# Optimization experiments

Measured on AMD Instinct MI355X. Metric: run time of the kernel, lower is better.

The kernel has to match this reference:

```python
import jax, jax.numpy as jnp
import numpy as np

B, S, HID = 4, 4096, 1024
NUM_HEADS, HEAD_DIM = 16, 64  # HID // NUM_HEADS
EPS = 1e-8  # torch F.cosine_similarity eps


def setup_inputs() -> dict:
    key = jax.random.key(0)
    ks = jax.random.split(key, 12)
    scale = 1.0 / np.sqrt(HID)
    d = {
        "query": jax.random.normal(ks[0], (B, S, HID), jnp.float32),
        "key": jax.random.normal(ks[1], (B, S, HID), jnp.float32),
        "value": jax.random.normal(ks[2], (B, S, HID), jnp.float32),
        "Wq": jax.random.normal(ks[3], (HID, HID), jnp.float32) * scale,
        "bq": jnp.zeros((HID,), jnp.float32),
        "Wk": jax.random.normal(ks[4], (HID, HID), jnp.float32) * scale,
        "bk": jnp.zeros((HID,), jnp.float32),
        "Wv": jax.random.normal(ks[5], (HID, HID), jnp.float32) * scale,
        "bv": jnp.zeros((HID,), jnp.float32),
        "Wo": jax.random.normal(ks[6], (HID, HID), jnp.float32) * scale,
        "bo": jnp.zeros((HID,), jnp.float32),
        "score_weights": jax.random.normal(ks[7], (3,), jnp.float32),
    }
    return d


def reference(query, key, value, Wq, bq, Wk, bk, Wv, bv, Wo, bo, score_weights):
    # Projections; NOTE: original reshapes to (B, S, H, D) and never transposes,
    # so all attention scores are over the HEADS axis (shape (B,S,H,H)).
    q = (query @ Wq + bq).reshape(B, S, NUM_HEADS, HEAD_DIM)
    k = (key @ Wk + bk).reshape(B, S, NUM_HEADS, HEAD_DIM)
    v = (value @ Wv + bv).reshape(B, S, NUM_HEADS, HEAD_DIM)

    # Shared inner products between heads at each (b, s): (B, S, H, H)
    qk = jnp.einsum('bsqd,bskd->bsqk', q, k)

    # 1) scaled dot product
    dot = qk / jnp.sqrt(jnp.float32(HEAD_DIM))

    # 2) cosine similarity (F.cosine_similarity with eps=1e-8)
    qn = jnp.linalg.norm(q, axis=-1)  # (B,S,H)
    kn = jnp.linalg.norm(k, axis=-1)
    cos = qk / jnp.maximum(qn[..., :, None] * kn[..., None, :], EPS)

    # 3) negative Euclidean distance (torch.cdist, p=2)
    sq = jnp.sum(q * q, axis=-1)  # (B,S,H)
    sk = jnp.sum(k * k, axis=-1)
    dist2 = jnp.maximum(sq[..., :, None] + sk[..., None, :] - 2.0 * qk, 0.0)
    dist = -jnp.sqrt(dist2)

    w = jax.nn.softmax(score_weights)
    scores = w[0] * dot + w[1] * cos + w[2] * dist  # (B,S,H,H)

    attention = jax.nn.softmax(scores, axis=-1)  # dropout = identity (eval)
    out = jnp.einsum('bsqk,bskd->bsqd', attention, v)  # (B,S,H,D)

    # Faithful to torch: transpose(1,2) -> (B,H,S,D), then view (B, S, HID)
    out = out.transpose(0, 2, 1, 3).reshape(B, S, HID)
    return out @ Wo + bo, attention
```

## Files before the change

kernel.cpp:

```cpp
#include <hip/hip_runtime.h>
#include <stdint.h>

#define BB 4
#define SS 4096
#define HID 1024
#define NH 16
#define HD 64
#define TOKENS (BB * SS)

typedef unsigned short u16;
typedef __bf16 bf16x8 __attribute__((ext_vector_type(8)));
typedef float f32x4 __attribute__((ext_vector_type(4)));
typedef __attribute__((address_space(1))) unsigned int u32g;
typedef __attribute__((address_space(3))) unsigned int u32l;

__device__ __forceinline__ u16 f2bf(float f) {
  union { float f; unsigned u; } v; v.f = f;
  unsigned u = v.u;
  unsigned r = u + 0x7fffu + ((u >> 16) & 1u);
  return (u16)(r >> 16);
}
__device__ __forceinline__ float bf2f(u16 h) {
  union { unsigned u; float f; } v; v.u = ((unsigned)h) << 16;
  return v.f;
}

__device__ __forceinline__ void async16(const void* g, void* l) {
  __builtin_amdgcn_global_load_lds((const u32g*)g, (u32l*)l, 16, 0, 0);
}

__global__ __launch_bounds__(256) void cast3_bf16(
    const float* __restrict__ q, const float* __restrict__ k,
    const float* __restrict__ v, u16* __restrict__ qo, u16* __restrict__ ko,
    u16* __restrict__ vo) {
  const int z = blockIdx.z;
  const float* s = (z == 0) ? q : (z == 1) ? k : v;
  u16* d = (z == 0) ? qo : (z == 1) ? ko : vo;
  size_t i = ((size_t)blockIdx.x * 256 + threadIdx.x) * 8;
  float4 f0 = *(const float4*)(s + i);
  float4 f1 = *(const float4*)(s + i + 4);
  ushort4 h0, h1;
  h0.x = f2bf(f0.x); h0.y = f2bf(f0.y); h0.z = f2bf(f0.z); h0.w = f2bf(f0.w);
  h1.x = f2bf(f1.x); h1.y = f2bf(f1.y); h1.z = f2bf(f1.z); h1.w = f2bf(f1.w);
  *(ushort4*)(d + i) = h0;
  *(ushort4*)(d + i + 4) = h1;
}

__global__ __launch_bounds__(256) void transpose_cast4(
    const float* __restrict__ W0, const float* __restrict__ W1,
    const float* __restrict__ W2, const float* __restrict__ W3,
    u16* __restrict__ T0, u16* __restrict__ T1, u16* __restrict__ T2,
    u16* __restrict__ T3) {
  const int z = blockIdx.z;
  const float* W = (z == 0) ? W0 : (z == 1) ? W1 : (z == 2) ? W2 : W3;
  u16* Wt = (z == 0) ? T0 : (z == 1) ? T1 : (z == 2) ? T2 : T3;
  __shared__ float t[32][33];
  const int bx = blockIdx.x * 32;
  const int by = blockIdx.y * 32;
  const int x = threadIdx.x;
#pragma unroll
  for (int yy = threadIdx.y; yy < 32; yy += 8)
    t[yy][x] = W[(size_t)(by + yy) * HID + bx + x];
  __syncthreads();
#pragma unroll
  for (int yy = threadIdx.y; yy < 32; yy += 8)
    Wt[(size_t)(bx + yy) * HID + by + x] = f2bf(t[x][yy]);
}

template <bool C_BF16, int NZ>
__global__ __launch_bounds__(256, 4) void gemm_bt(
    const u16* __restrict__ A0, const u16* __restrict__ A1,
    const u16* __restrict__ A2, const u16* __restrict__ B0,
    const u16* __restrict__ B1, const u16* __restrict__ B2,
    const float* __restrict__ bias0, const float* __restrict__ bias1,
    const float* __restrict__ bias2, void* __restrict__ C0,
    void* __restrict__ C1, void* __restrict__ C2, int M, int N, int K) {
  const u16* A = A0;
  const u16* Bt = B0;
  const float* bias = bias0;
  void* Cv = C0;
  if (NZ > 1) {
    int z = blockIdx.z;
    A = (z == 0) ? A0 : (z == 1) ? A1 : A2;
    Bt = (z == 0) ? B0 : (z == 1) ? B1 : B2;
    bias = (z == 0) ? bias0 : (z == 1) ? bias1 : bias2;
    Cv = (z == 0) ? C0 : (z == 1) ? C1 : C2;
  }
  __shared__ u16 As[128 * 32];
  __shared__ u16 Bs[128 * 32];
  const int tid = threadIdx.x;
  const int wave = tid >> 6, lane = tid & 63;
  const int quad = lane >> 4, l16 = lane & 15;
  const int m0 = blockIdx.x * 128, n0 = blockIdx.y * 128;
  const int wm = (wave >> 1) * 64, wn = (wave & 1) * 64;

  f32x4 acc[4][4] = {};

  for (int kt = 0; kt < K; kt += 32) {
    __syncthreads();
    {
      const u16* srcB = Bt + (size_t)n0 * K + kt;
      const u16* srcA = A + (size_t)m0 * K + kt;
#pragma unroll
      for (int is = 0; is < 2; ++is) {
        int g = is * 256 + wave * 64 + lane;
        const u16* gpB = srcB + (size_t)(g >> 2) * K + (g & 3) * 8;
        const u16* gpA = srcA + (size_t)(g >> 2) * K + (g & 3) * 8;
        async16(gpB, &Bs[(is * 256 + wave * 64) * 8]);
        async16(gpA, &As[(is * 256 + wave * 64) * 8]);
      }
    }
    __syncthreads();
    bf16x8 af[4], bfr[4];
#pragma unroll
    for (int i = 0; i < 4; ++i)
      af[i] = *(const bf16x8*)&As[(wm + i * 16 + l16) * 32 + quad * 8];
#pragma unroll
    for (int j = 0; j < 4; ++j)
      bfr[j] = *(const bf16x8*)&Bs[(wn + j * 16 + l16) * 32 + quad * 8];
#pragma unroll
    for (int i = 0; i < 4; ++i)
#pragma unroll
      for (int j = 0; j < 4; ++j)
        acc[i][j] = __builtin_amdgcn_mfma_f32_16x16x32_bf16(af[i], bfr[j],
                                                            acc[i][j], 0, 0, 0);
  }

  const int cb = n0 + wn + l16;
#pragma unroll
  for (int i = 0; i < 4; ++i) {
    int rowb = m0 + wm + i * 16 + quad * 4;
#pragma unroll
    for (int j = 0; j < 4; ++j) {
      int col = cb + j * 16;
      float bv = bias[col];
#pragma unroll
      for (int r = 0; r < 4; ++r) {
        float v = acc[i][j][r] + bv;
        if (C_BF16)
          ((u16*)Cv)[(size_t)(rowb + r) * N + col] = f2bf(v);
        else
          ((float*)Cv)[(size_t)(rowb + r) * N + col] = v;
      }
    }
  }
}

__global__ __launch_bounds__(256, 4) void attention_kernel(
    const u16* __restrict__ qb, const u16* __restrict__ kb,
    const u16* __restrict__ vb, const float* __restrict__ sw,
    float* __restrict__ attn_out, u16* __restrict__ o) {
  __shared__ float qs[16][65], ks[16][65], vs[16][65];
  __shared__ float sq[16], sk[16], qn[16], kn[16];
  __shared__ float attn_s[16][17];
  const int tid = threadIdx.x;
  const int token = blockIdx.x;
  const size_t base = (size_t)token * HID;

  {
    int idx = tid * 4;
    int h = idx >> 6, d = idx & 63;
    ushort4 uq = *(const ushort4*)(qb + base + idx);
    ushort4 uk = *(const ushort4*)(kb + base + idx);
    ushort4 uv = *(const ushort4*)(vb + base + idx);
    qs[h][d] = bf2f(uq.x); qs[h][d + 1] = bf2f(uq.y);
    qs[h][d + 2] = bf2f(uq.z); qs[h][d + 3] = bf2f(uq.w);
    ks[h][d] = bf2f(uk.x); ks[h][d + 1] = bf2f(uk.y);
    ks[h][d + 2] = bf2f(uk.z); ks[h][d + 3] = bf2f(uk.w);
    vs[h][d] = bf2f(uv.x); vs[h][d + 1] = bf2f(uv.y);
    vs[h][d + 2] = bf2f(uv.z); vs[h][d + 3] = bf2f(uv.w);
  }
  __syncthreads();

  if (tid < 32) {
    int i = tid & 15;
    const float* row = (tid < 16) ? qs[i] : ks[i];
    float s = 0.f;
#pragma unroll
    for (int d = 0; d < 64; ++d) s += row[d] * row[d];
    if (tid < 16) { sq[i] = s; qn[i] = sqrtf(s); }
    else          { sk[i] = s; kn[i] = sqrtf(s); }
  }
  __syncthreads();

  float s0 = sw[0], s1 = sw[1], s2 = sw[2];
  float smx = fmaxf(s0, fmaxf(s1, s2));
  float e0 = expf(s0 - smx), e1 = expf(s1 - smx), e2 = expf(s2 - smx);
  float winv = 1.f / (e0 + e1 + e2);
  float w0 = e0 * winv, w1 = e1 * winv, w2 = e2 * winv;

  const int i = tid >> 4, j = tid & 15;
  float attn;
  {
    float dot = 0.f;
#pragma unroll
    for (int d = 0; d < 64; ++d) dot += qs[i][d] * ks[j][d];
    float sdot = dot * 0.125f;
    float cosv = dot / fmaxf(qn[i] * kn[j], 1e-8f);
    float d2 = fmaxf(sq[i] + sk[j] - 2.f * dot, 0.f);
    float dist = -sqrtf(d2);
    float score = w0 * sdot + w1 * cosv + w2 * dist;
    float mx = score;
#pragma unroll
    for (int off = 8; off; off >>= 1) mx = fmaxf(mx, __shfl_xor(mx, off, 16));
    float e = expf(score - mx);
    float sum = e;
#pragma unroll
    for (int off = 8; off; off >>= 1) sum += __shfl_xor(sum, off, 16);
    attn = e / sum;
  }
  attn_out[(size_t)token * 256 + tid] = attn;
  attn_s[i][j] = attn;
  __syncthreads();

  {
    int d0 = j * 4;
    float o0 = 0.f, o1 = 0.f, o2 = 0.f, o3 = 0.f;
#pragma unroll
    for (int jj = 0; jj < 16; ++jj) {
      float a = attn_s[i][jj];
      o0 += a * vs[jj][d0];
      o1 += a * vs[jj][d0 + 1];
      o2 += a * vs[jj][d0 + 2];
      o3 += a * vs[jj][d0 + 3];
    }
    int b = token >> 12, s = token & (SS - 1);
    size_t off = (size_t)b * (SS * HID) + (size_t)i * (SS * HD) +
                 (size_t)s * HD + d0;
    ushort4 h;
    h.x = f2bf(o0); h.y = f2bf(o1); h.z = f2bf(o2); h.w = f2bf(o3);
    *(ushort4*)(o + off) = h;
  }
}

extern "C" void kernel_launch(void* const* d_in, const int* in_sizes, int n_in,
                              void* d_out, int out_size, void* d_ws,
                              size_t ws_size, hipStream_t stream) {
  (void)in_sizes; (void)n_in; (void)out_size; (void)ws_size;
  const float* query = (const float*)d_in[0];
  const float* key_  = (const float*)d_in[1];
  const float* value = (const float*)d_in[2];
  const float* Wq = (const float*)d_in[3];
  const float* bq = (const float*)d_in[4];
  const float* Wk = (const float*)d_in[5];
  const float* bk = (const float*)d_in[6];
  const float* Wv = (const float*)d_in[7];
  const float* bv = (const float*)d_in[8];
  const float* Wo = (const float*)d_in[9];
  const float* bo = (const float*)d_in[10];
  const float* sw = (const float*)d_in[11];

  char* ws = (char*)d_ws;
  u16* Wqt = (u16*)ws; ws += (size_t)HID * HID * 2;
  u16* Wkt = (u16*)ws; ws += (size_t)HID * HID * 2;
  u16* Wvt = (u16*)ws; ws += (size_t)HID * HID * 2;
  u16* Wot = (u16*)ws; ws += (size_t)HID * HID * 2;
  u16* qh = (u16*)ws; ws += (size_t)TOKENS * HID * 2;
  u16* kh = (u16*)ws; ws += (size_t)TOKENS * HID * 2;
  u16* vh = (u16*)ws; ws += (size_t)TOKENS * HID * 2;
  u16* qb = (u16*)ws; ws += (size_t)TOKENS * HID * 2;
  u16* kb = (u16*)ws; ws += (size_t)TOKENS * HID * 2;
  u16* vb = (u16*)ws; ws += (size_t)TOKENS * HID * 2;
  u16* ob = (u16*)ws; ws += (size_t)TOKENS * HID * 2;

  float* out0 = (float*)d_out;
  float* attn_out = out0 + (size_t)TOKENS * HID;

  transpose_cast4<<<dim3(32, 32, 4), dim3(32, 8), 0, stream>>>(
      Wq, Wk, Wv, Wo, Wqt, Wkt, Wvt, Wot);

  cast3_bf16<<<dim3(TOKENS * HID / (256 * 8), 1, 3), 256, 0, stream>>>(
      query, key_, value, qh, kh, vh);

  gemm_bt<true, 3><<<dim3(TOKENS / 128, HID / 128, 3), 256, 0, stream>>>(
      qh, kh, vh, Wqt, Wkt, Wvt, bq, bk, bv, qb, kb, vb, TOKENS, HID, HID);

  attention_kernel<<<TOKENS, 256, 0, stream>>>(qb, kb, vb, sw, attn_out, ob);

  gemm_bt<false, 1><<<dim3(TOKENS / 128, HID / 128, 1), 256, 0, stream>>>(
      ob, nullptr, nullptr, Wot, nullptr, nullptr, bo, nullptr, nullptr,
      out0, nullptr, nullptr, TOKENS, HID, HID);
}
```

Before: 506.7 us.

## Fuse input cast into QKV GEMM, swizzle LDS, MFMA-based per-token attention

Drops the separate fp32-to-bf16 cast kernel. The QKV GEMM now loads fp32 activations directly, converts them to bf16 in registers and writes them into XOR-swizzled LDS. Both GEMMs use the swizzled LDS layout to reduce bank conflicts. Attention processes four tokens per block, one per wave, computing the head-by-head QK product with MFMA and reusing the loaded fragments for the norms. It also uses fast exp and vectorized output stores. The trade-off is that the A tile is no longer loaded asynchronously into LDS, so global loads sit on the GEMM's critical path, and fast exp slightly changes numerics.

```diff
diff --git a/kernel.cpp b/kernel.cpp
--- a/kernel.cpp
+++ b/kernel.cpp
@@ -10,6 +10,7 @@
 
 typedef unsigned short u16;
 typedef __bf16 bf16x8 __attribute__((ext_vector_type(8)));
+typedef u16 u16x8 __attribute__((ext_vector_type(8)));
 typedef float f32x4 __attribute__((ext_vector_type(4)));
 typedef __attribute__((address_space(1))) unsigned int u32g;
 typedef __attribute__((address_space(3))) unsigned int u32l;
@@ -24,26 +25,12 @@
   union { unsigned u; float f; } v; v.u = ((unsigned)h) << 16;
   return v.f;
 }
+__device__ __forceinline__ unsigned pack2(float a, float b) {
+  return (unsigned)f2bf(a) | ((unsigned)f2bf(b) << 16);
+}
 
 __device__ __forceinline__ void async16(const void* g, void* l) {
   __builtin_amdgcn_global_load_lds((const u32g*)g, (u32l*)l, 16, 0, 0);
-}
-
-__global__ __launch_bounds__(256) void cast3_bf16(
-    const float* __restrict__ q, const float* __restrict__ k,
-    const float* __restrict__ v, u16* __restrict__ qo, u16* __restrict__ ko,
-    u16* __restrict__ vo) {
-  const int z = blockIdx.z;
-  const float* s = (z == 0) ? q : (z == 1) ? k : v;
-  u16* d = (z == 0) ? qo : (z == 1) ? ko : vo;
-  size_t i = ((size_t)blockIdx.x * 256 + threadIdx.x) * 8;
-  float4 f0 = *(const float4*)(s + i);
-  float4 f1 = *(const float4*)(s + i + 4);
-  ushort4 h0, h1;
-  h0.x = f2bf(f0.x); h0.y = f2bf(f0.y); h0.z = f2bf(f0.z); h0.w = f2bf(f0.w);
-  h1.x = f2bf(f1.x); h1.y = f2bf(f1.y); h1.z = f2bf(f1.z); h1.w = f2bf(f1.w);
-  *(ushort4*)(d + i) = h0;
-  *(ushort4*)(d + i + 4) = h1;
 }
 
 __global__ __launch_bounds__(256) void transpose_cast4(
@@ -67,25 +54,21 @@
     Wt[(size_t)(bx + yy) * HID + by + x] = f2bf(t[x][yy]);
 }
 
-template <bool C_BF16, int NZ>
-__global__ __launch_bounds__(256, 4) void gemm_bt(
-    const u16* __restrict__ A0, const u16* __restrict__ A1,
-    const u16* __restrict__ A2, const u16* __restrict__ B0,
+
+__global__ __launch_bounds__(256, 4) void gemm_qkv(
+    const float* __restrict__ A0, const float* __restrict__ A1,
+    const float* __restrict__ A2, const u16* __restrict__ B0,
     const u16* __restrict__ B1, const u16* __restrict__ B2,
     const float* __restrict__ bias0, const float* __restrict__ bias1,
-    const float* __restrict__ bias2, void* __restrict__ C0,
-    void* __restrict__ C1, void* __restrict__ C2, int M, int N, int K) {
-  const u16* A = A0;
-  const u16* Bt = B0;
-  const float* bias = bias0;
-  void* Cv = C0;
-  if (NZ > 1) {
-    int z = blockIdx.z;
-    A = (z == 0) ? A0 : (z == 1) ? A1 : A2;
-    Bt = (z == 0) ? B0 : (z == 1) ? B1 : B2;
-    bias = (z == 0) ? bias0 : (z == 1) ? bias1 : bias2;
-    Cv = (z == 0) ? C0 : (z == 1) ? C1 : C2;
-  }
+    const float* __restrict__ bias2, u16* __restrict__ C0,
+    u16* __restrict__ C1, u16* __restrict__ C2) {
+  const int z = blockIdx.z;
+  const float* A = (z == 0) ? A0 : (z == 1) ? A1 : A2;
+  const u16* Bt = (z == 0) ? B0 : (z == 1) ? B1 : B2;
+  const float* bias = (z == 0) ? bias0 : (z == 1) ? bias1 : bias2;
+  u16* Cv = (z == 0) ? C0 : (z == 1) ? C1 : C2;
+  const int K = HID, N = HID;
+
   __shared__ u16 As[128 * 32];
   __shared__ u16 Bs[128 * 32];
   const int tid = threadIdx.x;
@@ -93,6 +76,7 @@
   const int quad = lane >> 4, l16 = lane & 15;
   const int m0 = blockIdx.x * 128, n0 = blockIdx.y * 128;
   const int wm = (wave >> 1) * 64, wn = (wave & 1) * 64;
+  const int sw_frag = ((l16 >> 1) & 3);
 
   f32x4 acc[4][4] = {};
 
@@ -100,24 +84,42 @@
     __syncthreads();
     {
       const u16* srcB = Bt + (size_t)n0 * K + kt;
-      const u16* srcA = A + (size_t)m0 * K + kt;
 #pragma unroll
       for (int is = 0; is < 2; ++is) {
-        int g = is * 256 + wave * 64 + lane;
-        const u16* gpB = srcB + (size_t)(g >> 2) * K + (g & 3) * 8;
-        const u16* gpA = srcA + (size_t)(g >> 2) * K + (g & 3) * 8;
-        async16(gpB, &Bs[(is * 256 + wave * 64) * 8]);
-        async16(gpA, &As[(is * 256 + wave * 64) * 8]);
+        int slot = is * 256 + wave * 64 + lane;
+        int row = slot >> 2, c = slot & 3;
+        int cg = c ^ ((row >> 1) & 3);
+        async16(srcB + (size_t)row * K + cg * 8,
+                &Bs[(is * 256 + wave * 64) * 8]);
+      }
+    }
+    {
+      const float* srcA = A + (size_t)m0 * K + kt;
+#pragma unroll
+      for (int c2 = 0; c2 < 2; ++c2) {
+        int g = c2 * 256 + tid;
+        int row = g >> 2, cc = g & 3;
+        const float* gp = srcA + (size_t)row * K + cc * 8;
+        float4 f0 = *(const float4*)gp;
+        float4 f1 = *(const float4*)(gp + 4);
+        u16x8 h;
+        h[0] = f2bf(f0.x); h[1] = f2bf(f0.y); h[2] = f2bf(f0.z);
+        h[3] = f2bf(f0.w); h[4] = f2bf(f1.x); h[5] = f2bf(f1.y);
+        h[6] = f2bf(f1.z); h[7] = f2bf(f1.w);
+        int cs = cc ^ ((row >> 1) & 3);
+        *(u16x8*)&As[row * 32 + cs * 8] = h;
       }
     }
     __syncthreads();
     bf16x8 af[4], bfr[4];
 #pragma unroll
     for (int i = 0; i < 4; ++i)
-      af[i] = *(const bf16x8*)&As[(wm + i * 16 + l16) * 32 + quad * 8];
+      af[i] = *(const bf16x8*)&As[(wm + i * 16 + l16) * 32 +
+                                  (quad ^ sw_frag) * 8];
 #pragma unroll
     for (int j = 0; j < 4; ++j)
-      bfr[j] = *(const bf16x8*)&Bs[(wn + j * 16 + l16) * 32 + quad * 8];
+      bfr[j] = *(const bf16x8*)&Bs[(wn + j * 16 + l16) * 32 +
+                                   (quad ^ sw_frag) * 8];
 #pragma unroll
     for (int i = 0; i < 4; ++i)
 #pragma unroll
@@ -135,101 +137,181 @@
       int col = cb + j * 16;
       float bv = bias[col];
 #pragma unroll
-      for (int r = 0; r < 4; ++r) {
-        float v = acc[i][j][r] + bv;
-        if (C_BF16)
-          ((u16*)Cv)[(size_t)(rowb + r) * N + col] = f2bf(v);
-        else
-          ((float*)Cv)[(size_t)(rowb + r) * N + col] = v;
-      }
-    }
-  }
-}
-
-__global__ __launch_bounds__(256, 4) void attention_kernel(
+      for (int r = 0; r < 4; ++r)
+        Cv[(size_t)(rowb + r) * N + col] = f2bf(acc[i][j][r] + bv);
+    }
+  }
+}
+
+__global__ __launch_bounds__(256, 4) void gemm_ao(
+    const u16* __restrict__ A, const u16* __restrict__ Bt,
+    const float* __restrict__ bias, float* __restrict__ Cv) {
+  const int K = HID, N = HID;
+  __shared__ u16 As[128 * 32];
+  __shared__ u16 Bs[128 * 32];
+  const int tid = threadIdx.x;
+  const int wave = tid >> 6, lane = tid & 63;
+  const int quad = lane >> 4, l16 = lane & 15;
+  const int m0 = blockIdx.x * 128, n0 = blockIdx.y * 128;
+  const int wm = (wave >> 1) * 64, wn = (wave & 1) * 64;
+  const int sw_frag = ((l16 >> 1) & 3);
+
+  f32x4 acc[4][4] = {};
+
+  for (int kt = 0; kt < K; kt += 32) {
+    __syncthreads();
+    const u16* srcB = Bt + (size_t)n0 * K + kt;
+    const u16* srcA = A + (size_t)m0 * K + kt;
+#pragma unroll
+    for (int is = 0; is < 2; ++is) {
+      int slot = is * 256 + wave * 64 + lane;
+      int row = slot >> 2, c = slot & 3;
+      int cg = c ^ ((row >> 1) & 3);
+      async16(srcB + (size_t)row * K + cg * 8, &Bs[(is * 256 + wave * 64) * 8]);
+      async16(srcA + (size_t)row * K + cg * 8, &As[(is * 256 + wave * 64) * 8]);
+    }
+    __syncthreads();
+    bf16x8 af[4], bfr[4];
+#pragma unroll
+    for (int i = 0; i < 4; ++i)
+      af[i] = *(const bf16x8*)&As[(wm + i * 16 + l16) * 32 +
+                                  (quad ^ sw_frag) * 8];
+#pragma unroll
+    for (int j = 0; j < 4; ++j)
+      bfr[j] = *(const bf16x8*)&Bs[(wn + j * 16 + l16) * 32 +
+                                   (quad ^ sw_frag) * 8];
+#pragma unroll
+    for (int i = 0; i < 4; ++i)
+#pragma unroll
+      for (int j = 0; j < 4; ++j)
+        acc[i][j] = __builtin_amdgcn_mfma_f32_16x16x32_bf16(af[i], bfr[j],
+                                                            acc[i][j], 0, 0, 0);
+  }
+
+  const int cb = n0 + wn + l16;
+#pragma unroll
+  for (int i = 0; i < 4; ++i) {
+    int rowb = m0 + wm + i * 16 + quad * 4;
+#pragma unroll
+    for (int j = 0; j < 4; ++j) {
+      int col = cb + j * 16;
+      float bv = bias[col];
+#pragma unroll
+      for (int r = 0; r < 4; ++r)
+        Cv[(size_t)(rowb + r) * N + col] = acc[i][j][r] + bv;
+    }
+  }
+}
+
+__global__ __launch_bounds__(256) void attention_mfma(
     const u16* __restrict__ qb, const u16* __restrict__ kb,
     const u16* __restrict__ vb, const float* __restrict__ sw,
     float* __restrict__ attn_out, u16* __restrict__ o) {
-  __shared__ float qs[16][65], ks[16][65], vs[16][65];
-  __shared__ float sq[16], sk[16], qn[16], kn[16];
-  __shared__ float attn_s[16][17];
+  __shared__ float vs_s[4][16 * 68];
+  __shared__ float at_s[4][16 * 17];
   const int tid = threadIdx.x;
-  const int token = blockIdx.x;
+  const int wave = tid >> 6, lane = tid & 63;
+  const int quad = lane >> 4, l16 = lane & 15;
+  const int token = blockIdx.x * 4 + wave;
   const size_t base = (size_t)token * HID;
 
+  const u16* qp = qb + base + l16 * 64 + quad * 8;
+  const u16* kp = kb + base + l16 * 64 + quad * 8;
+  bf16x8 aq0 = *(const bf16x8*)qp;
+  bf16x8 aq1 = *(const bf16x8*)(qp + 32);
+  bf16x8 bk0 = *(const bf16x8*)kp;
+  bf16x8 bk1 = *(const bf16x8*)(kp + 32);
+
+  float* vsw = vs_s[wave];
   {
-    int idx = tid * 4;
-    int h = idx >> 6, d = idx & 63;
-    ushort4 uq = *(const ushort4*)(qb + base + idx);
-    ushort4 uk = *(const ushort4*)(kb + base + idx);
-    ushort4 uv = *(const ushort4*)(vb + base + idx);
-    qs[h][d] = bf2f(uq.x); qs[h][d + 1] = bf2f(uq.y);
-    qs[h][d + 2] = bf2f(uq.z); qs[h][d + 3] = bf2f(uq.w);
-    ks[h][d] = bf2f(uk.x); ks[h][d + 1] = bf2f(uk.y);
-    ks[h][d + 2] = bf2f(uk.z); ks[h][d + 3] = bf2f(uk.w);
-    vs[h][d] = bf2f(uv.x); vs[h][d + 1] = bf2f(uv.y);
-    vs[h][d + 2] = bf2f(uv.z); vs[h][d + 3] = bf2f(uv.w);
-  }
-  __syncthreads();
-
-  if (tid < 32) {
-    int i = tid & 15;
-    const float* row = (tid < 16) ? qs[i] : ks[i];
-    float s = 0.f;
-#pragma unroll
-    for (int d = 0; d < 64; ++d) s += row[d] * row[d];
-    if (tid < 16) { sq[i] = s; qn[i] = sqrtf(s); }
-    else          { sk[i] = s; kn[i] = sqrtf(s); }
-  }
-  __syncthreads();
+    const u16* vp = vb + base + lane * 16;
+    u16x8 h0 = *(const u16x8*)vp;
+    u16x8 h1 = *(const u16x8*)(vp + 8);
+    int row = lane >> 2, d0 = (lane & 3) * 16;
+    float* dst = vsw + row * 68 + d0;
+#pragma unroll
+    for (int c = 0; c < 8; ++c) { dst[c] = bf2f(h0[c]); dst[8 + c] = bf2f(h1[c]); }
+  }
+
+  f32x4 c = {};
+  c = __builtin_amdgcn_mfma_f32_16x16x32_bf16(aq0, bk0, c, 0, 0, 0);
+  c = __builtin_amdgcn_mfma_f32_16x16x32_bf16(aq1, bk1, c, 0, 0, 0);
+
+  float sq = 0.f, sk = 0.f;
+#pragma unroll
+  for (int jj = 0; jj < 8; ++jj) {
+    float a0 = (float)aq0[jj], a1 = (float)aq1[jj];
+    float b0 = (float)bk0[jj], b1 = (float)bk1[jj];
+    sq += a0 * a0 + a1 * a1;
+    sk += b0 * b0 + b1 * b1;
+  }
+  sq += __shfl_xor(sq, 16); sq += __shfl_xor(sq, 32);
+  sk += __shfl_xor(sk, 16); sk += __shfl_xor(sk, 32);
 
   float s0 = sw[0], s1 = sw[1], s2 = sw[2];
   float smx = fmaxf(s0, fmaxf(s1, s2));
-  float e0 = expf(s0 - smx), e1 = expf(s1 - smx), e2 = expf(s2 - smx);
+  float e0 = __expf(s0 - smx), e1 = __expf(s1 - smx), e2 = __expf(s2 - smx);
   float winv = 1.f / (e0 + e1 + e2);
   float w0 = e0 * winv, w1 = e1 * winv, w2 = e2 * winv;
 
-  const int i = tid >> 4, j = tid & 15;
-  float attn;
+  const float kn = sqrtf(sk);
+  float attn[4];
+#pragma unroll
+  for (int r = 0; r < 4; ++r) {
+    float sqr = __shfl(sq, (lane & 48) + quad * 4 + r);
+    float dot = c[r];
+    float sdot = dot * 0.125f;
+    float cosv = dot / fmaxf(sqrtf(sqr) * kn, 1e-8f);
+    float d2 = fmaxf(sqr + sk - 2.f * dot, 0.f);
+    float score = w0 * sdot + w1 * cosv - w2 * sqrtf(d2);
+    float mx = score;
+#pragma unroll
+    for (int off = 8; off; off >>= 1) mx = fmaxf(mx, __shfl_xor(mx, off, 16));
+    float e = __expf(score - mx);
+    float sum = e;
+#pragma unroll
+    for (int off = 8; off; off >>= 1) sum += __shfl_xor(sum, off, 16);
+    attn[r] = e / sum;
+  }
+
+  float* atw = at_s[wave];
+#pragma unroll
+  for (int r = 0; r < 4; ++r) {
+    int row = quad * 4 + r;
+    attn_out[(size_t)token * 256 + row * 16 + l16] = attn[r];
+    atw[row * 17 + l16] = attn[r];
+  }
+  __syncthreads();
+
+  float acc[16];
+#pragma unroll
+  for (int cc = 0; cc < 16; ++cc) acc[cc] = 0.f;
+  const int d0 = quad * 16;
+  const float* arow = atw + l16 * 17;
+#pragma unroll
+  for (int j = 0; j < 16; ++j) {
+    float a = arow[j];
+    const float* vr = vsw + j * 68 + d0;
+    float4 v0 = *(const float4*)vr;
+    float4 v1 = *(const float4*)(vr + 4);
+    float4 v2 = *(const float4*)(vr + 8);
+    float4 v3 = *(const float4*)(vr + 12);
+    acc[0] += a * v0.x;  acc[1] += a * v0.y;  acc[2] += a * v0.z;  acc[3] += a * v0.w;
+    acc[4] += a * v1.x;  acc[5] += a * v1.y;  acc[6] += a * v1.z;  acc[7] += a * v1.w;
+    acc[8] += a * v2.x;  acc[9] += a * v2.y;  acc[10] += a * v2.z; acc[11] += a * v2.w;
+    acc[12] += a * v3.x; acc[13] += a * v3.y; acc[14] += a * v3.z; acc[15] += a * v3.w;
+  }
   {
-    float dot = 0.f;
-#pragma unroll
-    for (int d = 0; d < 64; ++d) dot += qs[i][d] * ks[j][d];
-    float sdot = dot * 0.125f;
-    float cosv = dot / fmaxf(qn[i] * kn[j], 1e-8f);
-    float d2 = fmaxf(sq[i] + sk[j] - 2.f * dot, 0.f);
-    float dist = -sqrtf(d2);
-    float score = w0 * sdot + w1 * cosv + w2 * dist;
-    float mx = score;
-#pragma unroll
-    for (int off = 8; off; off >>= 1) mx = fmaxf(mx, __shfl_xor(mx, off, 16));
-    float e = expf(score - mx);
-    float sum = e;
-#pragma unroll
-    for (int off = 8; off; off >>= 1) sum += __shfl_xor(sum, off, 16);
-    attn = e / sum;
-  }
-  attn_out[(size_t)token * 256 + tid] = attn;
-  attn_s[i][j] = attn;
-  __syncthreads();
-
-  {
-    int d0 = j * 4;
-    float o0 = 0.f, o1 = 0.f, o2 = 0.f, o3 = 0.f;
-#pragma unroll
-    for (int jj = 0; jj < 16; ++jj) {
-      float a = attn_s[i][jj];
-      o0 += a * vs[jj][d0];
-      o1 += a * vs[jj][d0 + 1];
-      o2 += a * vs[jj][d0 + 2];
-      o3 += a * vs[jj][d0 + 3];
-    }
     int b = token >> 12, s = token & (SS - 1);
-    size_t off = (size_t)b * (SS * HID) + (size_t)i * (SS * HD) +
+    size_t off = (size_t)b * (SS * HID) + (size_t)l16 * (SS * HD) +
                  (size_t)s * HD + d0;
-    ushort4 h;
-    h.x = f2bf(o0); h.y = f2bf(o1); h.z = f2bf(o2); h.w = f2bf(o3);
-    *(ushort4*)(o + off) = h;
+    uint4 p0, p1;
+    p0.x = pack2(acc[0], acc[1]);   p0.y = pack2(acc[2], acc[3]);
+    p0.z = pack2(acc[4], acc[5]);   p0.w = pack2(acc[6], acc[7]);
+    p1.x = pack2(acc[8], acc[9]);   p1.y = pack2(acc[10], acc[11]);
+    p1.z = pack2(acc[12], acc[13]); p1.w = pack2(acc[14], acc[15]);
+    *(uint4*)(o + off) = p0;
+    *(uint4*)(o + off + 8) = p1;
   }
 }
 
@@ -255,9 +337,6 @@
   u16* Wkt = (u16*)ws; ws += (size_t)HID * HID * 2;
   u16* Wvt = (u16*)ws; ws += (size_t)HID * HID * 2;
   u16* Wot = (u16*)ws; ws += (size_t)HID * HID * 2;
-  u16* qh = (u16*)ws; ws += (size_t)TOKENS * HID * 2;
-  u16* kh = (u16*)ws; ws += (size_t)TOKENS * HID * 2;
-  u16* vh = (u16*)ws; ws += (size_t)TOKENS * HID * 2;
   u16* qb = (u16*)ws; ws += (size_t)TOKENS * HID * 2;
   u16* kb = (u16*)ws; ws += (size_t)TOKENS * HID * 2;
   u16* vb = (u16*)ws; ws += (size_t)TOKENS * HID * 2;
@@ -269,15 +348,11 @@
   transpose_cast4<<<dim3(32, 32, 4), dim3(32, 8), 0, stream>>>(
       Wq, Wk, Wv, Wo, Wqt, Wkt, Wvt, Wot);
 
-  cast3_bf16<<<dim3(TOKENS * HID / (256 * 8), 1, 3), 256, 0, stream>>>(
-      query, key_, value, qh, kh, vh);
-
-  gemm_bt<true, 3><<<dim3(TOKENS / 128, HID / 128, 3), 256, 0, stream>>>(
-      qh, kh, vh, Wqt, Wkt, Wvt, bq, bk, bv, qb, kb, vb, TOKENS, HID, HID);
-
-  attention_kernel<<<TOKENS, 256, 0, stream>>>(qb, kb, vb, sw, attn_out, ob);
-
-  gemm_bt<false, 1><<<dim3(TOKENS / 128, HID / 128, 1), 256, 0, stream>>>(
-      ob, nullptr, nullptr, Wot, nullptr, nullptr, bo, nullptr, nullptr,
-      out0, nullptr, nullptr, TOKENS, HID, HID);
-}
+  gemm_qkv<<<dim3(TOKENS / 128, HID / 128, 3), 256, 0, stream>>>(
+      query, key_, value, Wqt, Wkt, Wvt, bq, bk, bv, qb, kb, vb);
+
+  attention_mfma<<<TOKENS / 4, 256, 0, stream>>>(qb, kb, vb, sw, attn_out, ob);
+
+  gemm_ao<<<dim3(TOKENS / 128, HID / 128, 1), 256, 0, stream>>>(
+      ob, Wot, bo, out0);
+}
```

After: 462.9 us. 1.09x faster.
